# Kernel optimization log

Hardware: AMD Instinct MI355X
Metric: run time of the kernel (lower is better)

## Reference

```python
import jax, jax.numpy as jnp
import numpy as np

D_MODEL = 2048
D_FF = 8192


def _act_quant(x):
    # BitNet b1.58 per-token int8 absmax activation quantization with STE passthrough
    scale = 127.0 / jnp.clip(jnp.max(jnp.abs(x), axis=-1, keepdims=True), 1e-5)
    xq = jnp.clip(jnp.round(x * scale), -128.0, 127.0) / scale
    return x + jax.lax.stop_gradient(xq - x)


def _weight_quant(w):
    # Ternary {-1,0,1} weight quantization with per-tensor mean-abs scale
    scale = 1.0 / jnp.clip(jnp.mean(jnp.abs(w)), 1e-5)
    wq = jnp.clip(jnp.round(w * scale), -1.0, 1.0) / scale
    return w + jax.lax.stop_gradient(wq - w)


def _bitlinear(x, w):
    # y = Q_act(x) @ Q_w(w)^T   (w has shape [out, in], torch Linear convention)
    return jnp.einsum('bsd,fd->bsf', _act_quant(x), _weight_quant(w))


def setup_inputs() -> dict:
    key = jax.random.key(0)
    k_x, k_w1, k_w2 = jax.random.split(key, 3)
    x = jax.random.normal(k_x, (4, 4096, D_MODEL), dtype=jnp.float32)
    # torch Linear default init scale ~ 1/sqrt(fan_in)
    W1 = jax.random.normal(k_w1, (D_FF, D_MODEL), dtype=jnp.float32) / np.sqrt(D_MODEL)
    W2 = jax.random.normal(k_w2, (D_MODEL, D_FF), dtype=jnp.float32) / np.sqrt(D_FF)
    return {"x": x, "W1": W1, "W2": W2}


def reference(x, W1, W2):
    h = jax.nn.silu(_bitlinear(x, W1))   # [B, S, d_ff]
    return _bitlinear(h, W2)             # [B, S, d_model]; dropout p=0 -> identity
```

## Files before the change

### kernel.cpp

```cpp
#include <hip/hip_runtime.h>
#include <hip/hip_bf16.h>
#include <cstdint>

#define DM 2048
#define DF 8192

typedef int v4i __attribute__((ext_vector_type(4)));
typedef int v16i __attribute__((ext_vector_type(16)));
typedef short v8s __attribute__((ext_vector_type(8)));

__device__ __forceinline__ float silu_f(float y) {
  return y * (1.0f / (1.0f + expf(-y)));
}

__device__ __forceinline__ void gload_lds16(const void* g, void* l) {
  __builtin_amdgcn_global_load_lds(
      (const __attribute__((address_space(1))) void*)g,
      (__attribute__((address_space(3))) void*)l, 16, 0, 0);
}

__global__ __launch_bounds__(256) void abs_sum_k(const float* __restrict__ w,
                                                 float* __restrict__ partial) {
  const int t = threadIdx.x;
  const float4* wp = (const float4*)w;
  const long base = (long)blockIdx.x * 4096;
  float s = 0.f;
#pragma unroll
  for (int i = 0; i < 16; ++i) {
    float4 v = wp[base + i * 256 + t];
    s += fabsf(v.x) + fabsf(v.y) + fabsf(v.z) + fabsf(v.w);
  }
#pragma unroll
  for (int d = 1; d < 64; d <<= 1) s += __shfl_xor(s, d, 64);
  __shared__ float wsum[4];
  if ((t & 63) == 0) wsum[t >> 6] = s;
  __syncthreads();
  if (t == 0) partial[blockIdx.x] = (wsum[0] + wsum[1]) + (wsum[2] + wsum[3]);
}

__global__ __launch_bounds__(256) void finalize_scales_k(const float* __restrict__ p1,
                                                         const float* __restrict__ p2,
                                                         float* __restrict__ sc) {
  const float* p = (blockIdx.x == 0) ? p1 : p2;
  const int t = threadIdx.x;
  float s = (p[t] + p[t + 256]) + (p[t + 512] + p[t + 768]);
#pragma unroll
  for (int d = 1; d < 64; d <<= 1) s += __shfl_xor(s, d, 64);
  __shared__ float wsum[4];
  if ((t & 63) == 0) wsum[t >> 6] = s;
  __syncthreads();
  if (t == 0) {
    float total = (wsum[0] + wsum[1]) + (wsum[2] + wsum[3]);
    float mean = total * (1.0f / 16777216.0f);
    float c = fmaxf(mean, 1e-5f);
    sc[blockIdx.x * 2 + 0] = 1.0f / c;
    sc[blockIdx.x * 2 + 1] = c;
  }
}

__global__ __launch_bounds__(256) void tern_quant_k(const float* __restrict__ w,
                                                    int8_t* __restrict__ wq,
                                                    const float* __restrict__ scp) {
  const float s = scp[0];
  const long i = (long)blockIdx.x * 256 + threadIdx.x;
  float4 v = ((const float4*)w)[i];
  int q0 = (int)rintf(v.x * s); q0 = q0 < -1 ? -1 : (q0 > 1 ? 1 : q0);
  int q1 = (int)rintf(v.y * s); q1 = q1 < -1 ? -1 : (q1 > 1 ? 1 : q1);
  int q2 = (int)rintf(v.z * s); q2 = q2 < -1 ? -1 : (q2 > 1 ? 1 : q2);
  int q3 = (int)rintf(v.w * s); q3 = q3 < -1 ? -1 : (q3 > 1 ? 1 : q3);
  ((int*)wq)[i] = (q0 & 255) | ((q1 & 255) << 8) | ((q2 & 255) << 16) | ((q3 & 255) << 24);
}

__global__ __launch_bounds__(256) void act_quant_x_k(const float* __restrict__ x,
                                                     int8_t* __restrict__ xq,
                                                     float* __restrict__ inv_sx) {
  const int t = threadIdx.x;
  const long row = blockIdx.x;
  const float4* xr = (const float4*)(x + row * DM);
  float4 v0 = xr[t * 2], v1 = xr[t * 2 + 1];
  float m = fmaxf(fmaxf(fmaxf(fabsf(v0.x), fabsf(v0.y)), fmaxf(fabsf(v0.z), fabsf(v0.w))),
                  fmaxf(fmaxf(fabsf(v1.x), fabsf(v1.y)), fmaxf(fabsf(v1.z), fabsf(v1.w))));
#pragma unroll
  for (int d = 1; d < 64; d <<= 1) m = fmaxf(m, __shfl_xor(m, d, 64));
  __shared__ float wm[4];
  if ((t & 63) == 0) wm[t >> 6] = m;
  __syncthreads();
  m = fmaxf(fmaxf(wm[0], wm[1]), fmaxf(wm[2], wm[3]));
  const float scale = 127.0f / fmaxf(m, 1e-5f);
  if (t == 0) inv_sx[row] = 1.0f / scale;
  float vv[8] = {v0.x, v0.y, v0.z, v0.w, v1.x, v1.y, v1.z, v1.w};
  int q[8];
#pragma unroll
  for (int j = 0; j < 8; ++j) {
    int qq = (int)rintf(vv[j] * scale);
    q[j] = qq < -128 ? -128 : (qq > 127 ? 127 : qq);
  }
  int lo = (q[0] & 255) | ((q[1] & 255) << 8) | ((q[2] & 255) << 16) | ((q[3] & 255) << 24);
  int hi = (q[4] & 255) | ((q[5] & 255) << 8) | ((q[6] & 255) << 16) | ((q[7] & 255) << 24);
  ((int2*)(xq + row * DM))[t] = make_int2(lo, hi);
}

template <int MO>
__device__ __forceinline__ void cluster32(const v4i (&af)[2][4], const v4i (&bf)[2][4],
                                          v16i (&acc)[4][2]) {
  __builtin_amdgcn_s_setprio(1);
#pragma unroll
  for (int ks = 0; ks < 4; ++ks)
#pragma unroll
    for (int m = 0; m < 2; ++m)
#pragma unroll
      for (int n = 0; n < 2; ++n)
        acc[MO + m][n] = __builtin_amdgcn_mfma_i32_32x32x32_i8(
            af[m][ks], bf[n][ks], acc[MO + m][n], 0, 0, 0);
  __builtin_amdgcn_s_setprio(0);
}

template <int K, int N, int EPI>
__global__ __launch_bounds__(512, 2) void gemm8_i8_k(
    const int8_t* __restrict__ A, const int8_t* __restrict__ B,
    const float* __restrict__ rowInv, const float* __restrict__ invswp,
    short* __restrict__ Y16, float* __restrict__ Out) {
  constexpr int NT = K / 128;
  constexpr int NBX = N / 256;
  __shared__ __align__(16) uint8_t lds[131072];

  const int t = threadIdx.x;
  const int wave = t >> 6;
  const int lane = t & 63;
  const int wr = wave >> 2;
  const int wc = wave & 3;
  const int l31 = lane & 31, kg = lane >> 5;
  const int l15 = lane & 15, l4 = lane >> 4;

  const int cpx = (int)gridDim.x >> 3;
  const int bid0 = blockIdx.x;
  const int bid = (bid0 & 7) * cpx + (bid0 >> 3);
  const int bx = bid % NBX, by = bid / NBX;
  const long arow0 = (long)by * 256;
  const long bcol0 = (long)bx * 256;

  const int8_t* Ablk = A + arow0 * K;
  const int8_t* Bblk = B + bcol0 * K;

  const int srow = t >> 3;
  const int scol = ((t & 7) ^ (srow & 7)) << 4;

  const int rA = (wr * 128 + l31) * 128;
  const int rB = 32768 + (wc * 64 + l31) * 128;
  int cks[4];
#pragma unroll
  for (int ks = 0; ks < 4; ++ks) cks[ks] = (((ks << 1) | kg) ^ (l31 & 7)) << 4;

  v16i acc[4][2] = {};
  v4i a_lo[2][4], a_hi[2][4], b_all[2][4];

#define STAGE(ktile_, part_)                                                      \
  do {                                                                            \
    const int kk = (ktile_);                                                      \
    if (kk < NT) {                                                                \
      uint8_t* d0 = lds + ((kk & 1) << 16) + ((part_) << 14) + (wave << 10);      \
      const int8_t* sp = ((part_) < 2) ? Ablk : Bblk;                             \
      const int8_t* s0 =                                                          \
          sp + (long)((((part_) & 1) << 7) + srow) * K + ((long)kk << 7) + scol;  \
      gload_lds16(s0, d0);                                                        \
      gload_lds16(s0 + ((long)K << 6), d0 + 8192);                                \
    }                                                                             \
  } while (0)

#define SB __builtin_amdgcn_sched_barrier(0)
#define WAIT_LGKM8  asm volatile("s_waitcnt lgkmcnt(8)"  ::: "memory"); SB
#define WAIT_LGKM0  asm volatile("s_waitcnt lgkmcnt(0)"  ::: "memory"); SB
#define WAIT_VM4    asm volatile("s_waitcnt vmcnt(4)"    ::: "memory"); SB
#define WAIT_VM0    asm volatile("s_waitcnt vmcnt(0)"    ::: "memory"); SB

  STAGE(0, 0); STAGE(0, 1); STAGE(0, 2); STAGE(0, 3);
  STAGE(1, 0); STAGE(1, 1);
  WAIT_VM4;
  __builtin_amdgcn_s_barrier();
#pragma unroll
  for (int m = 0; m < 2; ++m)
#pragma unroll
    for (int ks = 0; ks < 4; ++ks)
      a_lo[m][ks] = *(const v4i*)(lds + rA + m * 4096 + cks[ks]);
  SB;

  for (int kt = 0; kt < NT; ++kt) {
    const uint8_t* sA = lds + ((kt & 1) << 16);
    const uint8_t* sB = sA;
    const uint8_t* sAn = lds + (((kt + 1) & 1) << 16);

#pragma unroll
    for (int n = 0; n < 2; ++n)
#pragma unroll
      for (int ks = 0; ks < 4; ++ks)
        b_all[n][ks] = *(const v4i*)(sB + rB + n * 4096 + cks[ks]);
    SB;
#pragma unroll
    for (int m = 0; m < 2; ++m)
#pragma unroll
      for (int ks = 0; ks < 4; ++ks)
        a_hi[m][ks] = *(const v4i*)(sA + rA + (m + 2) * 4096 + cks[ks]);
    SB;
    STAGE(kt + 1, 2);
    STAGE(kt + 1, 3);
    SB;
    WAIT_LGKM8;
    cluster32<0>(a_lo, b_all, acc);
    WAIT_VM4;
    WAIT_LGKM0;
    __builtin_amdgcn_s_barrier();
    if (kt + 1 < NT) {
#pragma unroll
      for (int m = 0; m < 2; ++m)
#pragma unroll
        for (int ks = 0; ks < 4; ++ks)
          a_lo[m][ks] = *(const v4i*)(sAn + rA + m * 4096 + cks[ks]);
      SB;
    }
    STAGE(kt + 2, 0);
    STAGE(kt + 2, 1);
    SB;
    cluster32<2>(a_hi, b_all, acc);
    if (kt < NT - 2) {
      WAIT_VM4;
    } else {
      WAIT_VM0;
    }
    __builtin_amdgcn_s_barrier();
  }

  if constexpr (EPI == 1) {
    __syncthreads();
#pragma unroll
    for (int mt = 0; mt < 4; ++mt) {
#pragma unroll
      for (int r = 0; r < 16; ++r) {
        const int row = wr * 128 + mt * 32 + (r & 3) + 8 * (r >> 2) + 4 * kg;
#pragma unroll
        for (int nt = 0; nt < 2; ++nt) {
          int yi = acc[mt][nt][r];
          int ys = yi < -32767 ? -32767 : (yi > 32767 ? 32767 : yi);
          const int col = wc * 64 + nt * 32 + l31;
          *(short*)(lds + ((row * 512 + col * 2) ^ ((row & 7) << 4))) = (short)ys;
        }
      }
    }
    __syncthreads();
    const int row = t >> 1;
    const int half = t & 1;
    short* gp = Y16 + (arow0 + row) * (long)DF + bcol0 + half * 128;
#pragma unroll
    for (int i = 0; i < 16; ++i) {
      v8s yv = *(const v8s*)(lds + ((row * 512 + half * 256 + i * 16) ^ ((row & 7) << 4)));
      *(v8s*)(gp + i * 8) = yv;
    }
  } else {
    const float invsw = invswp[0];
#pragma unroll
    for (int mt = 0; mt < 4; ++mt) {
#pragma unroll
      for (int r = 0; r < 16; ++r) {
        const long grow = arow0 + wr * 128 + mt * 32 + (r & 3) + 8 * (r >> 2) + 4 * kg;
        const float c2 = rowInv[grow] * invsw;
#pragma unroll
        for (int nt = 0; nt < 2; ++nt)
          Out[grow * N + bcol0 + wc * 64 + nt * 32 + l31] = (float)acc[mt][nt][r] * c2;
      }
    }
  }
#undef STAGE
#undef SB
#undef WAIT_LGKM8
#undef WAIT_LGKM0
#undef WAIT_VM4
#undef WAIT_VM0
}

__global__ __launch_bounds__(256) void quant_h_k(const short* __restrict__ Y16,
                                                 const float* __restrict__ inv_sx,
                                                 const float* __restrict__ sc,
                                                 int8_t* __restrict__ hq,
                                                 float* __restrict__ inv_sh) {
  const int t = threadIdx.x;
  const long row = blockIdx.x;
  const float c1 = inv_sx[row] * sc[1];
  const v8s* yp = (const v8s*)(Y16 + row * DF);
  float h[32];
  float mx = 0.f;
#pragma unroll
  for (int b = 0; b < 4; ++b) {
    v8s s8 = yp[b * 256 + t];
#pragma unroll
    for (int j = 0; j < 8; ++j) {
      float hv = silu_f((float)s8[j] * c1);
      h[b * 8 + j] = hv;
      mx = fmaxf(mx, fabsf(hv));
    }
  }
#pragma unroll
  for (int d = 1; d < 64; d <<= 1) mx = fmaxf(mx, __shfl_xor(mx, d, 64));
  __shared__ float wm[4];
  if ((t & 63) == 0) wm[t >> 6] = mx;
  __syncthreads();
  const float m = fmaxf(fmaxf(wm[0], wm[1]), fmaxf(wm[2], wm[3]));
  const float scale = 127.0f / fmaxf(m, 1e-5f);
  if (t == 0) inv_sh[row] = 1.0f / scale;
  int2* op = (int2*)(hq + row * DF);
#pragma unroll
  for (int b = 0; b < 4; ++b) {
    int q[8];
#pragma unroll
    for (int j = 0; j < 8; ++j) {
      int qq = (int)rintf(h[b * 8 + j] * scale);
      q[j] = qq < -128 ? -128 : (qq > 127 ? 127 : qq);
    }
    int lo = (q[0] & 255) | ((q[1] & 255) << 8) | ((q[2] & 255) << 16) | ((q[3] & 255) << 24);
    int hi = (q[4] & 255) | ((q[5] & 255) << 8) | ((q[6] & 255) << 16) | ((q[7] & 255) << 24);
    op[b * 256 + t] = make_int2(lo, hi);
  }
}

extern "C" void kernel_launch(void* const* d_in, const int* in_sizes, int n_in,
                              void* d_out, int out_size, void* d_ws, size_t ws_size,
                              hipStream_t stream) {
  const float* x = (const float*)d_in[0];
  const float* W1 = (const float*)d_in[1];
  const float* W2 = (const float*)d_in[2];
  float* out = (float*)d_out;

  uint8_t* w = (uint8_t*)d_ws;
  float* sc = (float*)(w + 0);
  float* p1 = (float*)(w + 256);
  float* p2 = (float*)(w + 256 + 4096);
  float* inv_sx = (float*)(w + 8448);
  float* inv_sh = (float*)(w + 8448 + 65536);
  uint8_t* w1q = w + 8448 + 131072 + 4194304;
  uint8_t* w2q = w1q + 16777216;
  uint8_t* xq = w2q + 16777216;
  uint8_t* hq = xq + 33554432;
  short* y16 = (short*)(hq + 134217728);

  abs_sum_k<<<1024, 256, 0, stream>>>(W1, p1);
  abs_sum_k<<<1024, 256, 0, stream>>>(W2, p2);
  finalize_scales_k<<<2, 256, 0, stream>>>(p1, p2, sc);
  tern_quant_k<<<16384, 256, 0, stream>>>(W1, (int8_t*)w1q, sc + 0);
  tern_quant_k<<<16384, 256, 0, stream>>>(W2, (int8_t*)w2q, sc + 2);
  act_quant_x_k<<<16384, 256, 0, stream>>>(x, (int8_t*)xq, inv_sx);
  gemm8_i8_k<2048, 8192, 1><<<2048, 512, 0, stream>>>(
      (const int8_t*)xq, (const int8_t*)w1q, nullptr, nullptr, y16, nullptr);
  quant_h_k<<<16384, 256, 0, stream>>>(y16, inv_sx, sc, (int8_t*)hq, inv_sh);
  gemm8_i8_k<8192, 2048, 0><<<512, 512, 0, stream>>>(
      (const int8_t*)hq, (const int8_t*)w2q, inv_sh, sc + 3, nullptr, out);
}
```

Baseline: 834.2 us.

## Batch weight-quant kernels over both weights and re-swizzle GEMM LDS layout

Merges the two abs-sum launches and the two ternary-quant launches into single 2D-grid launches covering W1 and W2, which removes some launch overhead and small-grid tails. It also changes the GEMM's global-to-LDS staging row mapping and the XOR swizzle used for reads: rows are interleaved in pairs with 256-byte stride, and the swizzle key now comes from the row-pair index. The aim is fewer LDS bank conflicts on the MFMA operand reads. The unseen load/compute code must still match the new rA/rB/cks offsets, or the results will be wrong.

```diff
diff --git a/kernel.cpp b/kernel.cpp
--- a/kernel.cpp
+++ b/kernel.cpp
@@ -19,9 +19,11 @@
       (__attribute__((address_space(3))) void*)l, 16, 0, 0);
 }
 
-__global__ __launch_bounds__(256) void abs_sum_k(const float* __restrict__ w,
+__global__ __launch_bounds__(256) void abs_sum_k(const float* __restrict__ w1,
+                                                 const float* __restrict__ w2,
                                                  float* __restrict__ partial) {
   const int t = threadIdx.x;
+  const float* w = blockIdx.y ? w2 : w1;
   const float4* wp = (const float4*)w;
   const long base = (long)blockIdx.x * 4096;
   float s = 0.f;
@@ -35,13 +37,12 @@
   __shared__ float wsum[4];
   if ((t & 63) == 0) wsum[t >> 6] = s;
   __syncthreads();
-  if (t == 0) partial[blockIdx.x] = (wsum[0] + wsum[1]) + (wsum[2] + wsum[3]);
-}
-
-__global__ __launch_bounds__(256) void finalize_scales_k(const float* __restrict__ p1,
-                                                         const float* __restrict__ p2,
+  if (t == 0) partial[blockIdx.y * 1024 + blockIdx.x] = (wsum[0] + wsum[1]) + (wsum[2] + wsum[3]);
+}
+
+__global__ __launch_bounds__(256) void finalize_scales_k(const float* __restrict__ partial,
                                                          float* __restrict__ sc) {
-  const float* p = (blockIdx.x == 0) ? p1 : p2;
+  const float* p = partial + blockIdx.x * 1024;
   const int t = threadIdx.x;
   float s = (p[t] + p[t + 256]) + (p[t + 512] + p[t + 768]);
 #pragma unroll
@@ -58,10 +59,14 @@
   }
 }
 
-__global__ __launch_bounds__(256) void tern_quant_k(const float* __restrict__ w,
-                                                    int8_t* __restrict__ wq,
-                                                    const float* __restrict__ scp) {
-  const float s = scp[0];
+__global__ __launch_bounds__(256) void tern_quant_k(const float* __restrict__ w1,
+                                                    const float* __restrict__ w2,
+                                                    int8_t* __restrict__ wq1,
+                                                    int8_t* __restrict__ wq2,
+                                                    const float* __restrict__ sc) {
+  const float* w = blockIdx.y ? w2 : w1;
+  int8_t* wq = blockIdx.y ? wq2 : wq1;
+  const float s = sc[blockIdx.y * 2];
   const long i = (long)blockIdx.x * 256 + threadIdx.x;
   float4 v = ((const float4*)w)[i];
   int q0 = (int)rintf(v.x * s); q0 = q0 < -1 ? -1 : (q0 > 1 ? 1 : q0);
@@ -130,7 +135,6 @@
   const int wr = wave >> 2;
   const int wc = wave & 3;
   const int l31 = lane & 31, kg = lane >> 5;
-  const int l15 = lane & 15, l4 = lane >> 4;
 
   const int cpx = (int)gridDim.x >> 3;
   const int bid0 = blockIdx.x;
@@ -142,14 +146,16 @@
   const int8_t* Ablk = A + arow0 * K;
   const int8_t* Bblk = B + bcol0 * K;
 
-  const int srow = t >> 3;
-  const int scol = ((t & 7) ^ (srow & 7)) << 4;
-
-  const int rA = (wr * 128 + l31) * 128;
-  const int rB = 32768 + (wc * 64 + l31) * 128;
+  const int srow = 2 * (t >> 4) + ((t >> 3) & 1);
+  const int scol = ((t & 7) ^ ((t >> 4) & 7)) << 4;
+
+  const int rb = (l31 >> 1) * 256 + (l31 & 1) * 128;
+  const int sx = (l31 >> 1) & 7;
+  const int rA = (wr << 14) + rb;
+  const int rB = 32768 + ((wc >> 1) << 14) + ((wc & 1) << 13) + rb;
   int cks[4];
 #pragma unroll
-  for (int ks = 0; ks < 4; ++ks) cks[ks] = (((ks << 1) | kg) ^ (l31 & 7)) << 4;
+  for (int ks = 0; ks < 4; ++ks) cks[ks] = (((ks << 1) | kg) ^ sx) << 4;
 
   v16i acc[4][2] = {};
   v4i a_lo[2][4], a_hi[2][4], b_all[2][4];
@@ -330,8 +336,7 @@
 
   uint8_t* w = (uint8_t*)d_ws;
   float* sc = (float*)(w + 0);
-  float* p1 = (float*)(w + 256);
-  float* p2 = (float*)(w + 256 + 4096);
+  float* partial = (float*)(w + 256);
   float* inv_sx = (float*)(w + 8448);
   float* inv_sh = (float*)(w + 8448 + 65536);
   uint8_t* w1q = w + 8448 + 131072 + 4194304;
@@ -340,11 +345,9 @@
   uint8_t* hq = xq + 33554432;
   short* y16 = (short*)(hq + 134217728);
 
-  abs_sum_k<<<1024, 256, 0, stream>>>(W1, p1);
-  abs_sum_k<<<1024, 256, 0, stream>>>(W2, p2);
-  finalize_scales_k<<<2, 256, 0, stream>>>(p1, p2, sc);
-  tern_quant_k<<<16384, 256, 0, stream>>>(W1, (int8_t*)w1q, sc + 0);
-  tern_quant_k<<<16384, 256, 0, stream>>>(W2, (int8_t*)w2q, sc + 2);
+  abs_sum_k<<<dim3(1024, 2), 256, 0, stream>>>(W1, W2, partial);
+  finalize_scales_k<<<2, 256, 0, stream>>>(partial, sc);
+  tern_quant_k<<<dim3(16384, 2), 256, 0, stream>>>(W1, W2, (int8_t*)w1q, (int8_t*)w2q, sc);
   act_quant_x_k<<<16384, 256, 0, stream>>>(x, (int8_t*)xq, inv_sx);
   gemm8_i8_k<2048, 8192, 1><<<2048, 512, 0, stream>>>(
       (const int8_t*)xq, (const int8_t*)w1q, nullptr, nullptr, y16, nullptr);
```

Result: no change. 840.2 us (+0.7%).
